# Optimization experiments

Measured on AMD Instinct MI355X. Metric: run time of the kernel, lower is better.

## Reference

```python
import jax, jax.numpy as jnp
import numpy as np

MASK_VALUE = -10000000.0

def reference(query, key, value, valid_length):
    # query: (B,n,d), key: (B,m,d), value: (B,m,dv), valid_length: (B,)
    d = key.shape[2]
    scale = 1.0 / jnp.sqrt(jnp.asarray(d, dtype=query.dtype))
    scores = jnp.einsum('bnd,bmd->bnm', query, key) * scale  # (B,n,m)
    m = key.shape[1]
    # mask positions >= valid_length per batch element
    mask = jnp.arange(m)[None, None, :] >= valid_length[:, None, None]  # (B,1,m)
    scores = jnp.where(mask, MASK_VALUE, scores)
    attn = jax.nn.softmax(scores, axis=-1)
    return jnp.einsum('bnm,bmv->bnv', attn, value)

def setup_inputs() -> dict:
    key = jax.random.key(0)
    k1, k2, k3, k4 = jax.random.split(key, 4)
    B, n, m, d, dv = 16, 1024, 1024, 128, 128
    return {
        'query': jax.random.normal(k1, (B, n, d), dtype=jnp.float32),
        'key': jax.random.normal(k2, (B, m, d), dtype=jnp.float32),
        'value': jax.random.normal(k3, (B, m, dv), dtype=jnp.float32),
        'valid_length': jax.random.randint(k4, (B,), 1, m + 1, dtype=jnp.int32),
    }
```

## Files before the change

kernel.cpp:

```cpp
#include <hip/hip_runtime.h>
#include <hip/hip_bf16.h>

typedef __attribute__((ext_vector_type(4))) float f32x4;
typedef __attribute__((ext_vector_type(8))) short s16x8;
typedef unsigned int u32;

#define DHEAD 128
#define KVBLK 64
#define BLKQ 64
#define TILEB 16384
#define PAIRB (2 * TILEB)

__device__ __forceinline__ short f2bf(float x) {
    __hip_bfloat16 h = __float2bfloat16(x);
    return *reinterpret_cast<short*>(&h);
}

__global__ __launch_bounds__(256)
void prep_frag(const float* __restrict__ K, const float* __restrict__ V,
               const float* __restrict__ Q, const int* __restrict__ VL,
               short* __restrict__ Kz, short* __restrict__ Vz, short* __restrict__ Qz,
               int m, int NT, int nkf, int nqf) {
    const int i = blockIdx.x * 256 + threadIdx.x;
    const float qsc = 0.08838834764831845f * 1.4426950408889634f;
    if (i < nkf) {
        const int lane = i & 63;
        const int kk   = (i >> 6) & 3;
        const int s    = (i >> 8) & 3;
        const int rest = i >> 10;
        const int t = rest % NT, b = rest / NT;
        if (t * KVBLK >= VL[b]) return;
        const int qi = lane & 15, g = lane >> 4;
        const float* src = K + (size_t)(b * m + t * KVBLK + 16 * s + qi) * DHEAD + kk * 32 + g * 8;
        f32x4 a = *reinterpret_cast<const f32x4*>(src);
        f32x4 c = *reinterpret_cast<const f32x4*>(src + 4);
        s16x8 o;
        #pragma unroll
        for (int j = 0; j < 4; ++j) { o[j] = f2bf(a[j]); o[4 + j] = f2bf(c[j]); }
        *reinterpret_cast<s16x8*>(Kz + (size_t)i * 8) = o;
    } else if (i < 2 * nkf) {
        const int j = i - nkf;
        const int lane = j & 63;
        const int kk   = (j >> 6) & 1;
        const int dg   = (j >> 7) & 7;
        const int rest = j >> 10;
        const int t = rest % NT, b = rest / NT;
        if (t * KVBLK >= VL[b]) return;
        const int qi = lane & 15, g = lane >> 4;
        const float* vb = V + (size_t)(b * m + t * KVBLK + kk * 32 + g * 4) * DHEAD + dg * 16 + qi;
        s16x8 o;
        #pragma unroll
        for (int r = 0; r < 4; ++r) {
            o[r]     = f2bf(vb[(size_t)r * DHEAD]);
            o[4 + r] = f2bf(vb[(size_t)(16 + r) * DHEAD]);
        }
        *reinterpret_cast<s16x8*>(Vz + (size_t)j * 8) = o;
    } else {
        const int j = i - 2 * nkf;
        if (j < nqf) {
            const int lane = j & 63;
            const int kk   = (j >> 6) & 3;
            const int grp  = j >> 8;
            const int qi = lane & 15, g = lane >> 4;
            const float* src = Q + ((size_t)grp * 16 + qi) * DHEAD + kk * 32 + g * 8;
            f32x4 a = *reinterpret_cast<const f32x4*>(src);
            f32x4 c = *reinterpret_cast<const f32x4*>(src + 4);
            s16x8 o;
            #pragma unroll
            for (int e = 0; e < 4; ++e) { o[e] = f2bf(a[e] * qsc); o[4 + e] = f2bf(c[e] * qsc); }
            *reinterpret_cast<s16x8*>(Qz + (size_t)j * 8) = o;
        }
    }
}

__global__ __launch_bounds__(256, 1)
void attn_fwd(const short* __restrict__ Qz, const short* __restrict__ Kz,
              const short* __restrict__ Vz, const int* __restrict__ VL,
              float* __restrict__ O, int B, int n, int NT) {
    __shared__ char lds[3 * PAIRB];

    const int tid  = threadIdx.x;
    const int lane = tid & 63;
    const int wid  = tid >> 6;
    const int g    = lane >> 4;
    const int qi   = lane & 15;

    const int nq = n / BLKQ;
    int b, qt;
    if ((B & 7) == 0) {
        const int xcd = blockIdx.x & 7;
        const int sub = blockIdx.x >> 3;
        const int bpx = B >> 3;
        b  = xcd * bpx + (sub % bpx);
        qt = sub / bpx;
    } else {
        b = blockIdx.x / nq; qt = blockIdx.x % nq;
    }

    const int vl = VL[b];
    const int nt = (vl + KVBLK - 1) >> 6;
    const int rowbase = b * n + qt * BLKQ + wid * 16;

    s16x8 qf[4];
    {
        const char* qg = (const char*)Qz + (size_t)(rowbase >> 4) * 4096 + lane * 16;
        #pragma unroll
        for (int kk = 0; kk < 4; ++kk)
            qf[kk] = *reinterpret_cast<const s16x8*>(qg + kk * 1024);
    }

    const char* KzB = (const char*)Kz + (size_t)b * NT * TILEB;
    const char* VzB = (const char*)Vz + (size_t)b * NT * TILEB;

    auto DMA = [&](int buf, int t) {
        const char* ks = KzB + (size_t)t * TILEB;
        const char* vs = VzB + (size_t)t * TILEB;
        char* dst = &lds[buf * PAIRB];
        #pragma unroll
        for (int j = 0; j < 4; ++j) {
            const int off = wid * 4096 + j * 1024;
            __builtin_amdgcn_global_load_lds(
                (const __attribute__((address_space(1))) u32*)(ks + off + lane * 16),
                (__attribute__((address_space(3))) u32*)(dst + off), 16, 0, 0);
            __builtin_amdgcn_global_load_lds(
                (const __attribute__((address_space(1))) u32*)(vs + off + lane * 16),
                (__attribute__((address_space(3))) u32*)(dst + TILEB + off), 16, 0, 0);
        }
    };

    f32x4 Oacc[8];
    #pragma unroll
    for (int dg = 0; dg < 8; ++dg) Oacc[dg] = 0.f;
    float llocal = 0.f;
    const int lb = lane * 16;

    DMA(0, 0);
    if (1 < nt) DMA(1, 1);

    int cur = 0;
    #pragma unroll 1
    for (int t = 0; t < nt; ++t) {
        if (t + 1 < nt) { asm volatile("s_waitcnt vmcnt(8)" ::: "memory"); }
        else            { asm volatile("s_waitcnt vmcnt(0)" ::: "memory"); }
        __builtin_amdgcn_s_barrier();

        if (t + 2 < nt) {
            int nb = cur + 2; if (nb >= 3) nb -= 3;
            DMA(nb, t + 2);
        }

        const char* ksb = &lds[cur * PAIRB];
        const char* vsb = ksb + TILEB;

        f32x4 Sacc[4];
        #pragma unroll
        for (int s = 0; s < 4; ++s) Sacc[s] = 0.f;
        __builtin_amdgcn_s_setprio(1);
        #pragma unroll
        for (int s = 0; s < 4; ++s)
            #pragma unroll
            for (int kk = 0; kk < 4; ++kk) {
                s16x8 kf = *reinterpret_cast<const s16x8*>(ksb + (s * 4 + kk) * 1024 + lb);
                Sacc[s] = __builtin_amdgcn_mfma_f32_16x16x32_bf16(kf, qf[kk], Sacc[s], 0, 0, 0);
            }
        __builtin_amdgcn_s_setprio(0);

        const int kvrem = vl - t * KVBLK;
        if (kvrem < KVBLK) {
            #pragma unroll
            for (int s = 0; s < 4; ++s)
                #pragma unroll
                for (int r = 0; r < 4; ++r)
                    if (s * 16 + g * 4 + r >= kvrem) Sacc[s][r] = -1e30f;
        }

        s16x8 pa[2];
        #pragma unroll
        for (int s = 0; s < 4; ++s)
            #pragma unroll
            for (int r = 0; r < 4; ++r) {
                const float e = __builtin_amdgcn_exp2f(fminf(Sacc[s][r], 60.f));
                llocal += e;
                pa[s >> 1][((s & 1) << 2) + r] = f2bf(e);
            }

        __builtin_amdgcn_s_setprio(1);
        #pragma unroll
        for (int dg = 0; dg < 8; ++dg)
            #pragma unroll
            for (int kk = 0; kk < 2; ++kk) {
                s16x8 vf = *reinterpret_cast<const s16x8*>(vsb + (dg * 2 + kk) * 1024 + lb);
                Oacc[dg] = __builtin_amdgcn_mfma_f32_16x16x32_bf16(pa[kk], vf, Oacc[dg], 0, 0, 0);
            }
        __builtin_amdgcn_s_setprio(0);

        cur += 1; if (cur >= 3) cur -= 3;
    }

    llocal += __shfl_xor(llocal, 16);
    llocal += __shfl_xor(llocal, 32);
    const float linv = 1.0f / llocal;
    const float l0 = __shfl(linv, g * 4 + 0);
    const float l1 = __shfl(linv, g * 4 + 1);
    const float l2 = __shfl(linv, g * 4 + 2);
    const float l3 = __shfl(linv, g * 4 + 3);
    float* Ob = O + (size_t)rowbase * DHEAD;
    #pragma unroll
    for (int dg = 0; dg < 8; ++dg) {
        Ob[(g * 4 + 0) * DHEAD + dg * 16 + qi] = Oacc[dg][0] * l0;
        Ob[(g * 4 + 1) * DHEAD + dg * 16 + qi] = Oacc[dg][1] * l1;
        Ob[(g * 4 + 2) * DHEAD + dg * 16 + qi] = Oacc[dg][2] * l2;
        Ob[(g * 4 + 3) * DHEAD + dg * 16 + qi] = Oacc[dg][3] * l3;
    }
}

extern "C" void kernel_launch(void* const* d_in, const int* in_sizes, int n_in,
                              void* d_out, int out_size, void* d_ws, size_t ws_size,
                              hipStream_t stream) {
    const float* Q  = (const float*)d_in[0];
    const float* K  = (const float*)d_in[1];
    const float* V  = (const float*)d_in[2];
    const int*   VL = (const int*)d_in[3];
    float* O = (float*)d_out;

    const int B = in_sizes[3];
    const int n = in_sizes[0] / (B * DHEAD);
    const int m = in_sizes[1] / (B * DHEAD);
    const int rows = B * n;
    const int NT = m / KVBLK;

    short* Kz = (short*)d_ws;
    short* Vz = Kz + (size_t)B * NT * (TILEB / 2);
    short* Qz = Vz + (size_t)B * NT * (TILEB / 2);

    const int nkf = B * NT * 1024;
    const int nqf = (rows / 16) * 256;
    prep_frag<<<(2 * nkf + nqf + 255) / 256, 256, 0, stream>>>(K, V, Q, VL, Kz, Vz, Qz, m, NT, nkf, nqf);

    const int grid = B * (n / BLKQ);
    attn_fwd<<<grid, 256, 0, stream>>>(Qz, Kz, Vz, VL, O, B, n, NT);
}
```

Before: 31.26 us.

## Fuse bf16 conversion into attention kernel, dropping the separate prep pass

The separate prep kernel that converted K, V and Q to bf16 fragment layout in workspace is removed. The attention kernel now loads fp32 Q/K/V directly, converts Q in registers, and stages K/V through registers into a double-buffered LDS layout, overlapping the loads for tile t+2 with compute on tile t. This avoids a kernel launch and the workspace write/read round trip. In exchange every query block re-reads and re-converts fp32 K/V (twice the bytes of bf16), which adds register pressure and conversion ALU work to the hot loop and replaces async direct-to-LDS DMA with register-staged copies.

```diff
diff --git a/kernel.cpp b/kernel.cpp
--- a/kernel.cpp
+++ b/kernel.cpp
@@ -3,7 +3,7 @@
 
 typedef __attribute__((ext_vector_type(4))) float f32x4;
 typedef __attribute__((ext_vector_type(8))) short s16x8;
-typedef unsigned int u32;
+typedef __attribute__((ext_vector_type(4))) short s16x4;
 
 #define DHEAD 128
 #define KVBLK 64
@@ -16,68 +16,11 @@
     return *reinterpret_cast<short*>(&h);
 }
 
-__global__ __launch_bounds__(256)
-void prep_frag(const float* __restrict__ K, const float* __restrict__ V,
-               const float* __restrict__ Q, const int* __restrict__ VL,
-               short* __restrict__ Kz, short* __restrict__ Vz, short* __restrict__ Qz,
-               int m, int NT, int nkf, int nqf) {
-    const int i = blockIdx.x * 256 + threadIdx.x;
-    const float qsc = 0.08838834764831845f * 1.4426950408889634f;
-    if (i < nkf) {
-        const int lane = i & 63;
-        const int kk   = (i >> 6) & 3;
-        const int s    = (i >> 8) & 3;
-        const int rest = i >> 10;
-        const int t = rest % NT, b = rest / NT;
-        if (t * KVBLK >= VL[b]) return;
-        const int qi = lane & 15, g = lane >> 4;
-        const float* src = K + (size_t)(b * m + t * KVBLK + 16 * s + qi) * DHEAD + kk * 32 + g * 8;
-        f32x4 a = *reinterpret_cast<const f32x4*>(src);
-        f32x4 c = *reinterpret_cast<const f32x4*>(src + 4);
-        s16x8 o;
-        #pragma unroll
-        for (int j = 0; j < 4; ++j) { o[j] = f2bf(a[j]); o[4 + j] = f2bf(c[j]); }
-        *reinterpret_cast<s16x8*>(Kz + (size_t)i * 8) = o;
-    } else if (i < 2 * nkf) {
-        const int j = i - nkf;
-        const int lane = j & 63;
-        const int kk   = (j >> 6) & 1;
-        const int dg   = (j >> 7) & 7;
-        const int rest = j >> 10;
-        const int t = rest % NT, b = rest / NT;
-        if (t * KVBLK >= VL[b]) return;
-        const int qi = lane & 15, g = lane >> 4;
-        const float* vb = V + (size_t)(b * m + t * KVBLK + kk * 32 + g * 4) * DHEAD + dg * 16 + qi;
-        s16x8 o;
-        #pragma unroll
-        for (int r = 0; r < 4; ++r) {
-            o[r]     = f2bf(vb[(size_t)r * DHEAD]);
-            o[4 + r] = f2bf(vb[(size_t)(16 + r) * DHEAD]);
-        }
-        *reinterpret_cast<s16x8*>(Vz + (size_t)j * 8) = o;
-    } else {
-        const int j = i - 2 * nkf;
-        if (j < nqf) {
-            const int lane = j & 63;
-            const int kk   = (j >> 6) & 3;
-            const int grp  = j >> 8;
-            const int qi = lane & 15, g = lane >> 4;
-            const float* src = Q + ((size_t)grp * 16 + qi) * DHEAD + kk * 32 + g * 8;
-            f32x4 a = *reinterpret_cast<const f32x4*>(src);
-            f32x4 c = *reinterpret_cast<const f32x4*>(src + 4);
-            s16x8 o;
-            #pragma unroll
-            for (int e = 0; e < 4; ++e) { o[e] = f2bf(a[e] * qsc); o[4 + e] = f2bf(c[e] * qsc); }
-            *reinterpret_cast<s16x8*>(Qz + (size_t)j * 8) = o;
-        }
-    }
-}
-
 __global__ __launch_bounds__(256, 1)
-void attn_fwd(const short* __restrict__ Qz, const short* __restrict__ Kz,
-              const short* __restrict__ Vz, const int* __restrict__ VL,
-              float* __restrict__ O, int B, int n, int NT) {
-    __shared__ char lds[3 * PAIRB];
+void attn_fwd(const float* __restrict__ Q, const float* __restrict__ K,
+              const float* __restrict__ V, const int* __restrict__ VL,
+              float* __restrict__ O, int B, int n, int m) {
+    __shared__ char lds[2 * PAIRB];
 
     const int tid  = threadIdx.x;
     const int lane = tid & 63;
@@ -101,31 +44,84 @@
     const int nt = (vl + KVBLK - 1) >> 6;
     const int rowbase = b * n + qt * BLKQ + wid * 16;
 
+    const float* Kb = K + (size_t)b * m * DHEAD;
+    const float* Vb = V + (size_t)b * m * DHEAD;
+
+    const float qsc = 0.08838834764831845f * 1.4426950408889634f;
     s16x8 qf[4];
     {
-        const char* qg = (const char*)Qz + (size_t)(rowbase >> 4) * 4096 + lane * 16;
-        #pragma unroll
-        for (int kk = 0; kk < 4; ++kk)
-            qf[kk] = *reinterpret_cast<const s16x8*>(qg + kk * 1024);
-    }
-
-    const char* KzB = (const char*)Kz + (size_t)b * NT * TILEB;
-    const char* VzB = (const char*)Vz + (size_t)b * NT * TILEB;
-
-    auto DMA = [&](int buf, int t) {
-        const char* ks = KzB + (size_t)t * TILEB;
-        const char* vs = VzB + (size_t)t * TILEB;
+        const float* qp = Q + ((size_t)rowbase + qi) * DHEAD + g * 8;
+        #pragma unroll
+        for (int kk = 0; kk < 4; ++kk) {
+            f32x4 a  = *reinterpret_cast<const f32x4*>(qp + kk * 32);
+            f32x4 cc = *reinterpret_cast<const f32x4*>(qp + kk * 32 + 4);
+            s16x8 s;
+            #pragma unroll
+            for (int j = 0; j < 4; ++j) { s[j] = f2bf(a[j] * qsc); s[4 + j] = f2bf(cc[j] * qsc); }
+            qf[kk] = s;
+        }
+    }
+
+    int krow[4], kcol[4];
+    #pragma unroll
+    for (int j = 0; j < 4; ++j) {
+        const int c  = tid + (j << 8);
+        const int lc = c & 63;
+        krow[j] = ((c >> 8) & 3) * 16 + (lc & 15);
+        kcol[j] = ((c >> 6) & 3) * 32 + (lc >> 4) * 8;
+    }
+    const int rq0 = tid >> 5;
+    const int dq  = tid & 31;
+    int vdst[2][4];
+    #pragma unroll
+    for (int p = 0; p < 2; ++p) {
+        const int rq = rq0 + 8 * p;
+        const int kk = rq >> 3, rem = rq & 7;
+        const int gw = rem & 3, half = rem >> 2;
+        #pragma unroll
+        for (int jj = 0; jj < 4; ++jj) {
+            const int dvr = dq * 4 + jj;
+            vdst[p][jj] = (((dvr >> 4) * 2 + kk) * 64 + gw * 16 + (dvr & 15)) * 16 + half * 8;
+        }
+    }
+
+    f32x4 kreg[8], vreg[8];
+    auto LOADK = [&](int t) {
+        const float* Kt = Kb + (size_t)t * KVBLK * DHEAD;
+        #pragma unroll
+        for (int j = 0; j < 4; ++j) {
+            const float* p = Kt + krow[j] * DHEAD + kcol[j];
+            kreg[2 * j]     = *reinterpret_cast<const f32x4*>(p);
+            kreg[2 * j + 1] = *reinterpret_cast<const f32x4*>(p + 4);
+        }
+    };
+    auto LOADV = [&](int t) {
+        const float* Vt = Vb + (size_t)t * KVBLK * DHEAD;
+        #pragma unroll
+        for (int p = 0; p < 2; ++p)
+            #pragma unroll
+            for (int r = 0; r < 4; ++r)
+                vreg[p * 4 + r] = *reinterpret_cast<const f32x4*>(Vt + ((rq0 + 8 * p) * 4 + r) * DHEAD + dq * 4);
+    };
+    auto CONV = [&](int buf) {
         char* dst = &lds[buf * PAIRB];
         #pragma unroll
         for (int j = 0; j < 4; ++j) {
-            const int off = wid * 4096 + j * 1024;
-            __builtin_amdgcn_global_load_lds(
-                (const __attribute__((address_space(1))) u32*)(ks + off + lane * 16),
-                (__attribute__((address_space(3))) u32*)(dst + off), 16, 0, 0);
-            __builtin_amdgcn_global_load_lds(
-                (const __attribute__((address_space(1))) u32*)(vs + off + lane * 16),
-                (__attribute__((address_space(3))) u32*)(dst + TILEB + off), 16, 0, 0);
-        }
+            s16x8 o;
+            #pragma unroll
+            for (int e = 0; e < 4; ++e) { o[e] = f2bf(kreg[2 * j][e]); o[4 + e] = f2bf(kreg[2 * j + 1][e]); }
+            *reinterpret_cast<s16x8*>(dst + (tid + (j << 8)) * 16) = o;
+        }
+        char* vb = dst + TILEB;
+        #pragma unroll
+        for (int p = 0; p < 2; ++p)
+            #pragma unroll
+            for (int jj = 0; jj < 4; ++jj) {
+                s16x4 sv;
+                sv[0] = f2bf(vreg[p * 4 + 0][jj]); sv[1] = f2bf(vreg[p * 4 + 1][jj]);
+                sv[2] = f2bf(vreg[p * 4 + 2][jj]); sv[3] = f2bf(vreg[p * 4 + 3][jj]);
+                *reinterpret_cast<s16x4*>(vb + vdst[p][jj]) = sv;
+            }
     };
 
     f32x4 Oacc[8];
@@ -134,21 +130,15 @@
     float llocal = 0.f;
     const int lb = lane * 16;
 
-    DMA(0, 0);
-    if (1 < nt) DMA(1, 1);
+    LOADK(0); LOADV(0);
+    CONV(0);
+    if (1 < nt) { LOADK(1); LOADV(1); }
+    asm volatile("s_waitcnt lgkmcnt(0)" ::: "memory");
+    __builtin_amdgcn_s_barrier();
 
     int cur = 0;
     #pragma unroll 1
     for (int t = 0; t < nt; ++t) {
-        if (t + 1 < nt) { asm volatile("s_waitcnt vmcnt(8)" ::: "memory"); }
-        else            { asm volatile("s_waitcnt vmcnt(0)" ::: "memory"); }
-        __builtin_amdgcn_s_barrier();
-
-        if (t + 2 < nt) {
-            int nb = cur + 2; if (nb >= 3) nb -= 3;
-            DMA(nb, t + 2);
-        }
-
         const char* ksb = &lds[cur * PAIRB];
         const char* vsb = ksb + TILEB;
 
@@ -184,6 +174,11 @@
                 pa[s >> 1][((s & 1) << 2) + r] = f2bf(e);
             }
 
+        if (t + 1 < nt) {
+            CONV(cur ^ 1);
+            if (t + 2 < nt) { LOADK(t + 2); LOADV(t + 2); }
+        }
+
         __builtin_amdgcn_s_setprio(1);
         #pragma unroll
         for (int dg = 0; dg < 8; ++dg)
@@ -194,7 +189,9 @@
             }
         __builtin_amdgcn_s_setprio(0);
 
-        cur += 1; if (cur >= 3) cur -= 3;
+        asm volatile("s_waitcnt lgkmcnt(0)" ::: "memory");
+        __builtin_amdgcn_s_barrier();
+        cur ^= 1;
     }
 
     llocal += __shfl_xor(llocal, 16);
@@ -226,17 +223,7 @@
     const int B = in_sizes[3];
     const int n = in_sizes[0] / (B * DHEAD);
     const int m = in_sizes[1] / (B * DHEAD);
-    const int rows = B * n;
-    const int NT = m / KVBLK;
-
-    short* Kz = (short*)d_ws;
-    short* Vz = Kz + (size_t)B * NT * (TILEB / 2);
-    short* Qz = Vz + (size_t)B * NT * (TILEB / 2);
-
-    const int nkf = B * NT * 1024;
-    const int nqf = (rows / 16) * 256;
-    prep_frag<<<(2 * nkf + nqf + 255) / 256, 256, 0, stream>>>(K, V, Q, VL, Kz, Vz, Qz, m, NT, nkf, nqf);
 
     const int grid = B * (n / BLKQ);
-    attn_fwd<<<grid, 256, 0, stream>>>(Qz, Kz, Vz, VL, O, B, n, NT);
+    attn_fwd<<<grid, 256, 0, stream>>>(Q, K, V, VL, O, B, n, m);
 }
```

New measurement: 34.93 us. 1.12x slower.
